# Kernel optimization log

Measured on AMD Instinct MI355X. Metric: run time of the kernel, lower is better.

## Reference

```python
import jax, jax.numpy as jnp
import numpy as np

N, D, H, O, E, K = 131072, 512, 512, 512, 8, 2
LN_EPS = 1e-5


def setup_inputs() -> dict:
    key = jax.random.key(0)
    k0, k1, k2, k3 = jax.random.split(key, 4)
    x = jax.random.normal(k0, (N, D), jnp.float32)
    # gate: nn.init.normal_(weight, 0, 0.1); stored as [D, E] (transposed torch layout)
    Wg = jax.random.normal(k1, (D, E), jnp.float32) * 0.1
    # experts: xavier_uniform for fc1/fc2, LayerNorm gamma=1, beta=0
    b1 = float(np.sqrt(6.0 / (D + H)))
    b2 = float(np.sqrt(6.0 / (H + O)))
    W1 = jax.random.uniform(k2, (E, D, H), jnp.float32, -b1, b1)
    W2 = jax.random.uniform(k3, (E, H, O), jnp.float32, -b2, b2)
    gamma = jnp.ones((E, H), jnp.float32)
    beta = jnp.zeros((E, H), jnp.float32)
    return {"x": x, "Wg": Wg, "W1": W1, "gamma": gamma, "beta": beta, "W2": W2}


def _layer_norm(h, g, b):
    mu = jnp.mean(h, axis=-1, keepdims=True)
    var = jnp.mean(jnp.square(h - mu), axis=-1, keepdims=True)  # biased, as torch LayerNorm
    return (h - mu) * jax.lax.rsqrt(var + LN_EPS) * g + b


def reference(x, Wg, W1, gamma, beta, W2):
    n = x.shape[0]
    # gating: softmax over experts (eval mode: no noise, no dropout)
    gating = jax.nn.softmax(x @ Wg, axis=-1)            # [N, E]
    vals, idx = jax.lax.top_k(gating, K)                # [N, K]
    # F.normalize(p=1): values are positive softmax probs -> divide by L1 sum
    vals = vals / jnp.maximum(jnp.sum(vals, axis=-1, keepdims=True), 1e-12)
    # scatter top-k weights into dense per-expert combine weights [N, E]
    cw = jnp.zeros((n, E), x.dtype).at[jnp.arange(n)[:, None], idx].add(vals)
    out = jnp.zeros((n, W2.shape[-1]), x.dtype)
    for e in range(E):  # small fixed loop over experts
        h = jax.nn.gelu(_layer_norm(x @ W1[e], gamma[e], beta[e]), approximate=False)
        out = out + cw[:, e:e + 1] * (h @ W2[e])
    return out
```

## Files before the change

kernel.cpp:

```cpp
#include <hip/hip_runtime.h>
#include <hip/hip_bf16.h>
#include <stdint.h>

#define NTOK 131072
#define NEXP 8

typedef unsigned short ushortT;
typedef __attribute__((ext_vector_type(4))) float f32x4;
typedef __attribute__((ext_vector_type(8))) short s16x8;
typedef __attribute__((ext_vector_type(8))) __bf16 bf16x8;

__device__ __forceinline__ float bfu2f(unsigned short u){
  union { float f; uint32_t i; } c; c.i = ((uint32_t)u) << 16; return c.f;
}
__device__ __forceinline__ unsigned short f2bfu(float f){
  union { float f; uint32_t i; } c; c.f = f;
  uint32_t x = c.i;
  uint32_t r = (x + 0x7fffu + ((x >> 16) & 1u)) >> 16;
  return (unsigned short)r;
}
__device__ __forceinline__ float gelu_f(float x){
  float u = 0.7978845608028654f * (x + 0.044715f * x * x * x);
  float e = __expf(2.0f * u);
  float t = 1.0f - 2.0f / (e + 1.0f);
  return 0.5f * x * (1.0f + t);
}
__device__ __forceinline__ bf16x8 ldfrag(const void* p){
  s16x8 v = *(const s16x8*)p;
  return __builtin_bit_cast(bf16x8, v);
}

__global__ __launch_bounds__(64) void zero_cursors_kernel(int* __restrict__ cursors){
  if (threadIdx.x < 16) cursors[threadIdx.x] = 0;
}

__global__ __launch_bounds__(256) void prep_w_kernel(const float* __restrict__ W1,
                                                     const float* __restrict__ W2,
                                                     ushortT* __restrict__ W1f,
                                                     ushortT* __restrict__ W2f){
  int bid = blockIdx.x;
  const float* src; ushortT* dst;
  if (bid < 512){ src = W1; dst = W1f; } else { src = W2; dst = W2f; bid -= 512; }
  int e  = bid >> 6;
  int kt = (bid >> 3) & 7;
  int nt = bid & 7;
  __shared__ ushortT tileT[64][68];
  int t = threadIdx.x;
  #pragma unroll
  for (int i = 0; i < 16; i++){
    int idx = t + i*256;
    int r = idx >> 6, c = idx & 63;
    float v = src[((size_t)(e*512 + kt*64 + r))*512 + nt*64 + c];
    tileT[c][r] = f2bfu(v);
  }
  __syncthreads();
  int sub = t >> 6, l = t & 63;
  #pragma unroll
  for (int fo = 0; fo < 2; fo++){
    int fr  = sub + fo*4;
    int nbl = fr >> 1;
    int ks  = fr & 1;
    int nb  = nt*4 + nbl;
    size_t fi = ((size_t)(e*32 + nb))*16 + kt*2 + ks;
    ushortT tmp[8];
    #pragma unroll
    for (int j = 0; j < 8; j++)
      tmp[j] = tileT[nbl*16 + (l & 15)][ks*32 + (l >> 4)*8 + j];
    *(s16x8*)(dst + fi*512 + l*8) = *(s16x8*)tmp;
  }
}

__global__ __launch_bounds__(256) void gating_kernel(const float* __restrict__ x,
                                                     const float* __restrict__ Wg,
                                                     ushortT* __restrict__ xbf,
                                                     int* __restrict__ epair,
                                                     float* __restrict__ wt){
  int l = threadIdx.x & 63;
  int wv = threadIdx.x >> 6;
  f32x4 wgv[16];
  #pragma unroll
  for (int i = 0; i < 8; i++){
    const f32x4* p = (const f32x4*)(Wg + (size_t)(l*8 + i)*8);
    wgv[2*i] = p[0]; wgv[2*i+1] = p[1];
  }
  int tbase = (blockIdx.x * 4 + wv) * 16;
  for (int tt = 0; tt < 16; tt++){
    int t = tbase + tt;
    const f32x4* xr = (const f32x4*)(x + (size_t)t*512 + l*8);
    f32x4 xa = xr[0], xb = xr[1];
    float acc[8];
    #pragma unroll
    for (int e2 = 0; e2 < 8; e2++) acc[e2] = 0.f;
    #pragma unroll
    for (int i = 0; i < 4; i++){
      float xi = xa[i], xj = xb[i];
      #pragma unroll
      for (int e2 = 0; e2 < 4; e2++){
        acc[e2]   += xi * wgv[2*i][e2];
        acc[4+e2] += xi * wgv[2*i+1][e2];
        acc[e2]   += xj * wgv[2*(i+4)][e2];
        acc[4+e2] += xj * wgv[2*(i+4)+1][e2];
      }
    }
    #pragma unroll
    for (int off = 1; off < 64; off <<= 1){
      #pragma unroll
      for (int e2 = 0; e2 < 8; e2++) acc[e2] += __shfl_xor(acc[e2], off);
    }
    int e0 = 0; float v0 = acc[0];
    #pragma unroll
    for (int e2 = 1; e2 < 8; e2++) if (acc[e2] > v0){ v0 = acc[e2]; e0 = e2; }
    int e1 = -1; float v1 = -3.4e38f;
    #pragma unroll
    for (int e2 = 0; e2 < 8; e2++){ if (e2 != e0 && acc[e2] > v1){ v1 = acc[e2]; e1 = e2; } }
    float w0 = 1.f / (1.f + __expf(v1 - v0));
    if (l == 0){
      epair[t] = e0 | (e1 << 4);
      wt[t] = w0;
      wt[NTOK + t] = 1.f - w0;
    }
    s16x8 o;
    #pragma unroll
    for (int j = 0; j < 4; j++){ o[j] = (short)f2bfu(xa[j]); o[4+j] = (short)f2bfu(xb[j]); }
    *(s16x8*)(xbf + (size_t)t*512 + l*8) = o;
  }
}

__global__ __launch_bounds__(256) void scatter_kernel(const int* __restrict__ epair,
                                                      int* __restrict__ cursors,
                                                      int* __restrict__ lists){
  __shared__ int cntL[16]; __shared__ int baseL[16];
  int tid = threadIdx.x;
  if (tid < 16) cntL[tid] = 0;
  __syncthreads();
  int t = blockIdx.x * 256 + tid;
  int p = epair[t];
  int e0 = p & 15, e1 = (p >> 4) & 15;
  int lp0 = atomicAdd(&cntL[e0], 1);
  int lp1 = atomicAdd(&cntL[8 + e1], 1);
  __syncthreads();
  if (tid < 16) baseL[tid] = atomicAdd(&cursors[tid], cntL[tid]);
  __syncthreads();
  lists[(size_t)e0 * NTOK + baseL[e0] + lp0] = t;
  lists[(size_t)(8 + e1) * NTOK + baseL[8 + e1] + lp1] = t;
}

template<int SLOT>
__global__ __launch_bounds__(512, 2) void expert_kernel(
    const ushortT* __restrict__ xbf, const ushortT* __restrict__ W1bf,
    const ushortT* __restrict__ W2bf, const float* __restrict__ gamma,
    const float* __restrict__ beta, const float* __restrict__ wt,
    const int* __restrict__ cursors, const int* __restrict__ lists,
    float* __restrict__ out)
{
  __shared__ ushortT hX[64 * 512];
  __shared__ int   toksL[64];
  __shared__ float wrowL[64];
  __shared__ float wsumL[8][64];
  __shared__ float wsqL[8][64];
  __shared__ float muL[64];
  __shared__ float rsL[64];

  int tid = threadIdx.x;
  int w = tid >> 6;
  int l = tid & 63;

  int bid = (int)blockIdx.x;
  bid = (bid & 7) * 257 + (bid >> 3);

  int e = -1, tile = 0, bacc = 0, cn = 0;
  #pragma unroll
  for (int i = 0; i < 8; i++){
    int c = cursors[SLOT*8 + i];
    int ntl = (c + 63) >> 6;
    if (e < 0 && bid < bacc + ntl){ e = i; tile = bid - bacc; cn = c; }
    bacc += ntl;
  }
  if (e < 0) return;
  int tb = tile * 64;

  if (tid < 64){
    int idx = tb + tid;
    int tok = (idx < cn) ? lists[(size_t)(SLOT*8 + e) * NTOK + idx] : -1;
    toksL[tid] = tok;
    wrowL[tid] = (tok >= 0) ? wt[(size_t)SLOT*NTOK + tok] : 0.f;
  }
  __syncthreads();

  {
    int r = tid >> 3, cs = tid & 7;
    int tokS = toksL[r]; if (tokS < 0) tokS = toksL[0];
    const int4* xrow = (const int4*)(xbf + (size_t)tokS * 512);
    int4 xv[8];
    #pragma unroll
    for (int i = 0; i < 8; i++) xv[i] = xrow[cs + i*8];
    #pragma unroll
    for (int i = 0; i < 8; i++){
      int slot = cs + i*8;
      int ss = slot ^ (r & 7);
      *(int4*)((char*)hX + r*1024 + ss*16) = xv[i];
    }
  }
  __syncthreads();

  const ushortT* w1f = W1bf + ((size_t)(e*32 + w*4))*16*512;
  f32x4 acc[4][4];
  #pragma unroll
  for (int m = 0; m < 4; m++)
    #pragma unroll
    for (int nf = 0; nf < 4; nf++) acc[m][nf] = (f32x4){0.f,0.f,0.f,0.f};

  #pragma unroll 2
  for (int kt = 0; kt < 8; kt++){
    #pragma unroll
    for (int ks = 0; ks < 2; ks++){
      bf16x8 A[4];
      #pragma unroll
      for (int m = 0; m < 4; m++){
        int row = (l & 15) + m*16;
        int slot = kt*8 + ks*4 + (l >> 4);
        A[m] = ldfrag((const char*)hX + row*1024 + (slot ^ (row & 7))*16);
      }
      #pragma unroll
      for (int nf = 0; nf < 4; nf++){
        bf16x8 B = ldfrag(w1f + ((size_t)(nf*16 + kt*2 + ks))*512 + l*8);
        #pragma unroll
        for (int m = 0; m < 4; m++)
          acc[m][nf] = __builtin_amdgcn_mfma_f32_16x16x32_bf16(A[m], B, acc[m][nf], 0, 0, 0);
      }
    }
  }

  #pragma unroll
  for (int m = 0; m < 4; m++){
    #pragma unroll
    for (int j = 0; j < 4; j++){
      float s = acc[m][0][j] + acc[m][1][j] + acc[m][2][j] + acc[m][3][j];
      float q = acc[m][0][j]*acc[m][0][j] + acc[m][1][j]*acc[m][1][j]
              + acc[m][2][j]*acc[m][2][j] + acc[m][3][j]*acc[m][3][j];
      s += __shfl_xor(s, 1); q += __shfl_xor(q, 1);
      s += __shfl_xor(s, 2); q += __shfl_xor(q, 2);
      s += __shfl_xor(s, 4); q += __shfl_xor(q, 4);
      s += __shfl_xor(s, 8); q += __shfl_xor(q, 8);
      if ((l & 15) == 0){
        int row = m*16 + (l >> 4)*4 + j;
        wsumL[w][row] = s;
        wsqL[w][row]  = q;
      }
    }
  }
  __syncthreads();

  if (tid < 64){
    float s = 0.f, q = 0.f;
    #pragma unroll
    for (int i = 0; i < 8; i++){ s += wsumL[i][tid]; q += wsqL[i][tid]; }
    float mu = s * (1.f/512.f);
    float var = q * (1.f/512.f) - mu*mu;
    muL[tid] = mu;
    rsL[tid] = rsqrtf(var + 1e-5f);
  }
  __syncthreads();

  {
    float g[4], b[4];
    #pragma unroll
    for (int nf = 0; nf < 4; nf++){
      int col = w*64 + nf*16 + (l & 15);
      g[nf] = gamma[e*512 + col];
      b[nf] = beta [e*512 + col];
    }
    #pragma unroll
    for (int m = 0; m < 4; m++){
      #pragma unroll
      for (int j = 0; j < 4; j++){
        int row = m*16 + (l >> 4)*4 + j;
        float mu = muL[row], rs = rsL[row];
        #pragma unroll
        for (int nf = 0; nf < 4; nf++){
          int col = w*64 + nf*16 + (l & 15);
          float v = (acc[m][nf][j] - mu) * rs * g[nf] + b[nf];
          v = gelu_f(v);
          int ss = (col >> 3) ^ (row & 7);
          *(ushortT*)((char*)hX + row*1024 + ss*16 + (col & 7)*2) = f2bfu(v);
        }
      }
    }
  }
  __syncthreads();

  const ushortT* w2f = W2bf + ((size_t)(e*32 + w*4))*16*512;
  #pragma unroll
  for (int m = 0; m < 4; m++)
    #pragma unroll
    for (int nf = 0; nf < 4; nf++) acc[m][nf] = (f32x4){0.f,0.f,0.f,0.f};

  #pragma unroll 2
  for (int kt = 0; kt < 8; kt++){
    #pragma unroll
    for (int ks = 0; ks < 2; ks++){
      bf16x8 A[4];
      #pragma unroll
      for (int m = 0; m < 4; m++){
        int row = (l & 15) + m*16;
        int slot = kt*8 + ks*4 + (l >> 4);
        A[m] = ldfrag((const char*)hX + row*1024 + (slot ^ (row & 7))*16);
      }
      #pragma unroll
      for (int nf = 0; nf < 4; nf++){
        bf16x8 B = ldfrag(w2f + ((size_t)(nf*16 + kt*2 + ks))*512 + l*8);
        #pragma unroll
        for (int m = 0; m < 4; m++)
          acc[m][nf] = __builtin_amdgcn_mfma_f32_16x16x32_bf16(A[m], B, acc[m][nf], 0, 0, 0);
      }
    }
  }

  #pragma unroll
  for (int m = 0; m < 4; m++){
    #pragma unroll
    for (int j = 0; j < 4; j++){
      int row = m*16 + (l >> 4)*4 + j;
      int tok = toksL[row];
      if (tok >= 0){
        float wr = wrowL[row];
        #pragma unroll
        for (int nf = 0; nf < 4; nf++){
          int col = w*64 + nf*16 + (l & 15);
          float val = acc[m][nf][j] * wr;
          float* p = out + (size_t)tok*512 + col;
          if (SLOT == 0) *p = val; else *p += val;
        }
      }
    }
  }
}

extern "C" void kernel_launch(void* const* d_in, const int* in_sizes, int n_in,
                              void* d_out, int out_size, void* d_ws, size_t ws_size,
                              hipStream_t stream){
  const float* x     = (const float*)d_in[0];
  const float* Wg    = (const float*)d_in[1];
  const float* W1    = (const float*)d_in[2];
  const float* gamma = (const float*)d_in[3];
  const float* beta  = (const float*)d_in[4];
  const float* W2    = (const float*)d_in[5];
  float* out = (float*)d_out;

  char* ws = (char*)d_ws;
  size_t off = 0;
  ushortT* xbf   = (ushortT*)(ws + off); off += (size_t)NTOK*512*2;
  ushortT* W1bf  = (ushortT*)(ws + off); off += (size_t)8*512*512*2;
  ushortT* W2bf  = (ushortT*)(ws + off); off += (size_t)8*512*512*2;
  int*     lists = (int*)(ws + off);     off += (size_t)16*NTOK*4;
  float*   wtp   = (float*)(ws + off);   off += (size_t)2*NTOK*4;
  int*     epair = (int*)(ws + off);     off += (size_t)NTOK*4;
  int*     cursors = (int*)(ws + off);   off += 256;

  zero_cursors_kernel<<<1, 64, 0, stream>>>(cursors);
  prep_w_kernel<<<1024, 256, 0, stream>>>(W1, W2, W1bf, W2bf);
  gating_kernel<<<NTOK/64, 256, 0, stream>>>(x, Wg, xbf, epair, wtp);
  scatter_kernel<<<NTOK/256, 256, 0, stream>>>(epair, cursors, lists);
  expert_kernel<0><<<2056, 512, 0, stream>>>(xbf, W1bf, W2bf, gamma, beta, wtp, cursors, lists, out);
  expert_kernel<1><<<2056, 512, 0, stream>>>(xbf, W1bf, W2bf, gamma, beta, wtp, cursors, lists, out);
}
```

Measured before the change: 639.8 us.

## Raise expert kernel occupancy and double-buffer weight fragment loads in GEMMs

Raises launch bounds from 2 to 4 blocks per CU. Both expert GEMMs become fully unrolled loops that prefetch the next step's B fragments from global memory while the current MFMAs run, using precomputed swizzled LDS offsets. The token gather now reads the list directly instead of waiting on a barrier after the shared token table is filled, and gamma/beta are loaded per use rather than held in registers. Doubling occupancy caps registers per thread more tightly, which may cause spills given the 64-float accumulator plus double-buffered fragments. LDS use of about 64KB per block may also keep four blocks from fitting on a CU.

```diff
diff --git a/kernel.cpp b/kernel.cpp
--- a/kernel.cpp
+++ b/kernel.cpp
@@ -146,7 +146,7 @@
 }
 
 template<int SLOT>
-__global__ __launch_bounds__(512, 2) void expert_kernel(
+__global__ __launch_bounds__(512, 4) void expert_kernel(
     const ushortT* __restrict__ xbf, const ushortT* __restrict__ W1bf,
     const ushortT* __restrict__ W2bf, const float* __restrict__ gamma,
     const float* __restrict__ beta, const float* __restrict__ wt,
@@ -178,56 +178,75 @@
   }
   if (e < 0) return;
   int tb = tile * 64;
+  const int* lbase = lists + (size_t)(SLOT*8 + e) * NTOK;
 
   if (tid < 64){
     int idx = tb + tid;
-    int tok = (idx < cn) ? lists[(size_t)(SLOT*8 + e) * NTOK + idx] : -1;
+    int tok = (idx < cn) ? lbase[idx] : -1;
     toksL[tid] = tok;
     wrowL[tid] = (tok >= 0) ? wt[(size_t)SLOT*NTOK + tok] : 0.f;
   }
-  __syncthreads();
 
   {
     int r = tid >> 3, cs = tid & 7;
-    int tokS = toksL[r]; if (tokS < 0) tokS = toksL[0];
+    int idx = tb + r; if (idx >= cn) idx = tb;
+    int tokS = lbase[idx];
     const int4* xrow = (const int4*)(xbf + (size_t)tokS * 512);
-    int4 xv[8];
-    #pragma unroll
-    for (int i = 0; i < 8; i++) xv[i] = xrow[cs + i*8];
-    #pragma unroll
-    for (int i = 0; i < 8; i++){
-      int slot = cs + i*8;
-      int ss = slot ^ (r & 7);
-      *(int4*)((char*)hX + r*1024 + ss*16) = xv[i];
-    }
-  }
-  __syncthreads();
+    #pragma unroll
+    for (int half = 0; half < 2; half++){
+      int4 xv[4];
+      #pragma unroll
+      for (int i = 0; i < 4; i++) xv[i] = xrow[cs + (half*4 + i)*8];
+      #pragma unroll
+      for (int i = 0; i < 4; i++){
+        int slot = cs + (half*4 + i)*8;
+        int ss = slot ^ (r & 7);
+        *(int4*)((char*)hX + r*1024 + ss*16) = xv[i];
+      }
+    }
+  }
+  __syncthreads();
+
+  const int aB0 = (l & 15)*1024 + ((((l >> 4)    ) ^ (l & 7)) << 4);
+  const int aB1 = (l & 15)*1024 + (((4 + (l >> 4)) ^ (l & 7)) << 4);
+  const char* Xp = (const char*)hX;
 
   const ushortT* w1f = W1bf + ((size_t)(e*32 + w*4))*16*512;
+  const ushortT* w2f = W2bf + ((size_t)(e*32 + w*4))*16*512;
+
   f32x4 acc[4][4];
+
+#define LOADB(dst, wf, s_) { \
+    _Pragma("unroll") \
+    for (int nf = 0; nf < 4; nf++) \
+      dst[nf] = ldfrag((wf) + ((nf*16 + (s_)) << 9) + (l << 3)); }
+#define LOADA(dst, s_) { \
+    const int ab_ = ((s_) & 1) ? aB1 : aB0; \
+    _Pragma("unroll") \
+    for (int m = 0; m < 4; m++) \
+      dst[m] = ldfrag(Xp + ab_ + m*16384 + ((s_) >> 1)*128); }
+#define MFMAS(Aa, Bb) { \
+    _Pragma("unroll") \
+    for (int nf = 0; nf < 4; nf++) \
+      _Pragma("unroll") \
+      for (int m = 0; m < 4; m++) \
+        acc[m][nf] = __builtin_amdgcn_mfma_f32_16x16x32_bf16(Aa[m], Bb[nf], acc[m][nf], 0, 0, 0); }
+
   #pragma unroll
   for (int m = 0; m < 4; m++)
     #pragma unroll
     for (int nf = 0; nf < 4; nf++) acc[m][nf] = (f32x4){0.f,0.f,0.f,0.f};
-
-  #pragma unroll 2
-  for (int kt = 0; kt < 8; kt++){
-    #pragma unroll
-    for (int ks = 0; ks < 2; ks++){
-      bf16x8 A[4];
-      #pragma unroll
-      for (int m = 0; m < 4; m++){
-        int row = (l & 15) + m*16;
-        int slot = kt*8 + ks*4 + (l >> 4);
-        A[m] = ldfrag((const char*)hX + row*1024 + (slot ^ (row & 7))*16);
-      }
-      #pragma unroll
-      for (int nf = 0; nf < 4; nf++){
-        bf16x8 B = ldfrag(w1f + ((size_t)(nf*16 + kt*2 + ks))*512 + l*8);
-        #pragma unroll
-        for (int m = 0; m < 4; m++)
-          acc[m][nf] = __builtin_amdgcn_mfma_f32_16x16x32_bf16(A[m], B, acc[m][nf], 0, 0, 0);
-      }
+  {
+    bf16x8 Ba[4], Bb[4];
+    LOADB(Ba, w1f, 0);
+    #pragma unroll
+    for (int s = 0; s < 16; s += 2){
+      { bf16x8 A[4]; LOADA(A, s);
+        LOADB(Bb, w1f, s+1);
+        MFMAS(A, Ba); }
+      { bf16x8 A[4]; LOADA(A, s+1);
+        if (s+2 < 16) LOADB(Ba, w1f, s+2);
+        MFMAS(A, Bb); }
     }
   }
 
@@ -263,13 +282,6 @@
   __syncthreads();
 
   {
-    float g[4], b[4];
-    #pragma unroll
-    for (int nf = 0; nf < 4; nf++){
-      int col = w*64 + nf*16 + (l & 15);
-      g[nf] = gamma[e*512 + col];
-      b[nf] = beta [e*512 + col];
-    }
     #pragma unroll
     for (int m = 0; m < 4; m++){
       #pragma unroll
@@ -279,7 +291,9 @@
         #pragma unroll
         for (int nf = 0; nf < 4; nf++){
           int col = w*64 + nf*16 + (l & 15);
-          float v = (acc[m][nf][j] - mu) * rs * g[nf] + b[nf];
+          float g = gamma[e*512 + col];
+          float b = beta [e*512 + col];
+          float v = (acc[m][nf][j] - mu) * rs * g + b;
           v = gelu_f(v);
           int ss = (col >> 3) ^ (row & 7);
           *(ushortT*)((char*)hX + row*1024 + ss*16 + (col & 7)*2) = f2bfu(v);
@@ -289,30 +303,21 @@
   }
   __syncthreads();
 
-  const ushortT* w2f = W2bf + ((size_t)(e*32 + w*4))*16*512;
   #pragma unroll
   for (int m = 0; m < 4; m++)
     #pragma unroll
     for (int nf = 0; nf < 4; nf++) acc[m][nf] = (f32x4){0.f,0.f,0.f,0.f};
-
-  #pragma unroll 2
-  for (int kt = 0; kt < 8; kt++){
-    #pragma unroll
-    for (int ks = 0; ks < 2; ks++){
-      bf16x8 A[4];
-      #pragma unroll
-      for (int m = 0; m < 4; m++){
-        int row = (l & 15) + m*16;
-        int slot = kt*8 + ks*4 + (l >> 4);
-        A[m] = ldfrag((const char*)hX + row*1024 + (slot ^ (row & 7))*16);
-      }
-      #pragma unroll
-      for (int nf = 0; nf < 4; nf++){
-        bf16x8 B = ldfrag(w2f + ((size_t)(nf*16 + kt*2 + ks))*512 + l*8);
-        #pragma unroll
-        for (int m = 0; m < 4; m++)
-          acc[m][nf] = __builtin_amdgcn_mfma_f32_16x16x32_bf16(A[m], B, acc[m][nf], 0, 0, 0);
-      }
+  {
+    bf16x8 Ba[4], Bb[4];
+    LOADB(Ba, w2f, 0);
+    #pragma unroll
+    for (int s = 0; s < 16; s += 2){
+      { bf16x8 A[4]; LOADA(A, s);
+        LOADB(Bb, w2f, s+1);
+        MFMAS(A, Ba); }
+      { bf16x8 A[4]; LOADA(A, s+1);
+        if (s+2 < 16) LOADB(Ba, w2f, s+2);
+        MFMAS(A, Bb); }
     }
   }
 
@@ -334,6 +339,9 @@
       }
     }
   }
+#undef LOADB
+#undef LOADA
+#undef MFMAS
 }
 
 extern "C" void kernel_launch(void* const* d_in, const int* in_sizes, int n_in,
```

Result: slower. 748.4 us (+17.0%).

## Split fused expert kernel into tiled GEMM1, LayerNorm-GELU, and GEMM2 passes

Applied to the files above, without the earlier changes.

Replaces the single fused per-expert kernel with three kernels. The first GEMM is tiled 128 rows x 128 cols with double-buffered direct global-to-LDS loads, and it writes raw bf16 activations plus partial row statistics to a workspace. A separate kernel applies LayerNorm and GELU in place. A second tiled GEMM reads the activations back and scatters the weighted output. The aim is better operand reuse, load/compute overlap and occupancy, paid for by extra HBM round-trips of the hidden activations and more kernel launches.

```diff
diff --git a/kernel.cpp b/kernel.cpp
--- a/kernel.cpp
+++ b/kernel.cpp
@@ -4,6 +4,7 @@
 
 #define NTOK 131072
 #define NEXP 8
+#define HPAD 132096
 
 typedef unsigned short ushortT;
 typedef __attribute__((ext_vector_type(4))) float f32x4;
@@ -29,6 +30,10 @@
   s16x8 v = *(const s16x8*)p;
   return __builtin_bit_cast(bf16x8, v);
 }
+
+#define GLOAD16(g_, l_) \
+  __builtin_amdgcn_global_load_lds((const __attribute__((address_space(1))) uint32_t*)(g_), \
+                                   (__attribute__((address_space(3))) uint32_t*)(l_), 16, 0, 0)
 
 __global__ __launch_bounds__(64) void zero_cursors_kernel(int* __restrict__ cursors){
   if (threadIdx.x < 16) cursors[threadIdx.x] = 0;
@@ -146,188 +151,253 @@
 }
 
 template<int SLOT>
-__global__ __launch_bounds__(512, 2) void expert_kernel(
+__global__ __launch_bounds__(256, 3) void g1_kernel(
     const ushortT* __restrict__ xbf, const ushortT* __restrict__ W1bf,
-    const ushortT* __restrict__ W2bf, const float* __restrict__ gamma,
-    const float* __restrict__ beta, const float* __restrict__ wt,
     const int* __restrict__ cursors, const int* __restrict__ lists,
-    float* __restrict__ out)
+    ushortT* __restrict__ hraw, float* __restrict__ stats)
 {
-  __shared__ ushortT hX[64 * 512];
-  __shared__ int   toksL[64];
-  __shared__ float wrowL[64];
-  __shared__ float wsumL[8][64];
-  __shared__ float wsqL[8][64];
-  __shared__ float muL[64];
-  __shared__ float rsL[64];
-
-  int tid = threadIdx.x;
-  int w = tid >> 6;
-  int l = tid & 63;
-
-  int bid = (int)blockIdx.x;
-  bid = (bid & 7) * 257 + (bid >> 3);
+  __shared__ ushortT Abuf[2][4096];
+  __shared__ ushortT Bbuf[2][4096];
+  __shared__ int toksL[128];
+
+  int tid = threadIdx.x, w = tid >> 6, l = tid & 63;
+  int braw = (int)blockIdx.x;
+  int bid = (braw & 7)*516 + (braw >> 3);
+  int t128 = bid >> 2, nt = bid & 3;
 
   int e = -1, tile = 0, bacc = 0, cn = 0;
   #pragma unroll
   for (int i = 0; i < 8; i++){
     int c = cursors[SLOT*8 + i];
-    int ntl = (c + 63) >> 6;
-    if (e < 0 && bid < bacc + ntl){ e = i; tile = bid - bacc; cn = c; }
+    int ntl = (c + 127) >> 7;
+    if (e < 0 && t128 < bacc + ntl){ e = i; tile = t128 - bacc; cn = c; }
     bacc += ntl;
   }
   if (e < 0) return;
-  int tb = tile * 64;
-
+  const int* lbase = lists + (size_t)(SLOT*8 + e) * NTOK;
+
+  if (tid < 128){
+    int idx = tile*128 + tid;
+    toksL[tid] = lbase[(idx < cn) ? idx : tile*128];
+  }
+  __syncthreads();
+
+  int rA0 = tid >> 2, rA1 = 64 + (tid >> 2), cA = tid & 3;
+  int swzA = (cA ^ (rA0 & 3)) << 4;
+  const char* srcA0 = (const char*)(xbf + (size_t)toksL[rA0]*512) + swzA;
+  const char* srcA1 = (const char*)(xbf + (size_t)toksL[rA1]*512) + swzA;
+  const char* srcB0 = (const char*)W1bf + ((size_t)((e*32 + nt*8 + w    )*16))*1024 + (l << 4);
+  const char* srcB1 = (const char*)W1bf + ((size_t)((e*32 + nt*8 + w + 4)*16))*1024 + (l << 4);
+
+#define STAGE_(b_, s_) { \
+    GLOAD16(srcA0 + (size_t)(s_)*64,   &Abuf[b_][w*512]); \
+    GLOAD16(srcA1 + (size_t)(s_)*64,   &Abuf[b_][2048 + w*512]); \
+    GLOAD16(srcB0 + (size_t)(s_)*1024, &Bbuf[b_][w*512]); \
+    GLOAD16(srcB1 + (size_t)(s_)*1024, &Bbuf[b_][2048 + w*512]); }
+
+  int wr = w >> 1, wc = w & 1;
+  int aswz = ((l >> 4) ^ (l & 3)) << 4;
+  int ab0 = (wr*64 + (l & 15))*64 + aswz;
+  int bb0 = (wc*4)*1024 + (l << 4);
+
+  f32x4 acc[4][4];
+  #pragma unroll
+  for (int m = 0; m < 4; m++)
+    #pragma unroll
+    for (int nf = 0; nf < 4; nf++) acc[m][nf] = (f32x4){0.f,0.f,0.f,0.f};
+
+  STAGE_(0, 0);
+  __syncthreads();
+  for (int s = 0; s < 16; s++){
+    int b = s & 1;
+    if (s < 15) STAGE_(b ^ 1, s + 1);
+    bf16x8 A[4], B[4];
+    #pragma unroll
+    for (int m = 0; m < 4; m++)  A[m]  = ldfrag((const char*)&Abuf[b][0] + ab0 + m*1024);
+    #pragma unroll
+    for (int nf = 0; nf < 4; nf++) B[nf] = ldfrag((const char*)&Bbuf[b][0] + bb0 + nf*1024);
+    #pragma unroll
+    for (int nf = 0; nf < 4; nf++)
+      #pragma unroll
+      for (int m = 0; m < 4; m++)
+        acc[m][nf] = __builtin_amdgcn_mfma_f32_16x16x32_bf16(A[m], B[nf], acc[m][nf], 0, 0, 0);
+    __syncthreads();
+  }
+#undef STAGE_
+
+  #pragma unroll
+  for (int m = 0; m < 4; m++){
+    #pragma unroll
+    for (int j = 0; j < 4; j++){
+      float s1 = acc[m][0][j] + acc[m][1][j] + acc[m][2][j] + acc[m][3][j];
+      float q1 = acc[m][0][j]*acc[m][0][j] + acc[m][1][j]*acc[m][1][j]
+               + acc[m][2][j]*acc[m][2][j] + acc[m][3][j]*acc[m][3][j];
+      s1 += __shfl_xor(s1, 1); q1 += __shfl_xor(q1, 1);
+      s1 += __shfl_xor(s1, 2); q1 += __shfl_xor(q1, 2);
+      s1 += __shfl_xor(s1, 4); q1 += __shfl_xor(q1, 4);
+      s1 += __shfl_xor(s1, 8); q1 += __shfl_xor(q1, 8);
+      int r = wr*64 + m*16 + (l >> 4)*4 + j;
+      int i = tile*128 + r;
+      if (i < cn){
+        size_t grow = (size_t)t128*128 + r;
+        if ((l & 15) == 0){
+          float2 v; v.x = s1; v.y = q1;
+          *((float2*)stats + grow*8 + (nt*2 + wc)) = v;
+        }
+        #pragma unroll
+        for (int nf = 0; nf < 4; nf++)
+          hraw[grow*512 + nt*128 + wc*64 + nf*16 + (l & 15)] = f2bfu(acc[m][nf][j]);
+      }
+    }
+  }
+}
+
+template<int SLOT>
+__global__ __launch_bounds__(256) void lng_kernel(
+    const int* __restrict__ cursors, const float* __restrict__ stats,
+    const float* __restrict__ gamma, const float* __restrict__ beta,
+    ushortT* __restrict__ hraw)
+{
+  __shared__ float gL[512], bL[512], muL[64], rsL[64];
+  int tid = threadIdx.x;
+  int braw = (int)blockIdx.x;
+  int t64 = (braw & 7)*258 + (braw >> 3);
+  int e = -1, bacc = 0, tstart = 0, cn = 0;
+  #pragma unroll
+  for (int i = 0; i < 8; i++){
+    int c = cursors[SLOT*8 + i];
+    int ntl = 2*((c + 127) >> 7);
+    if (e < 0 && t64 < bacc + ntl){ e = i; tstart = bacc; cn = c; }
+    bacc += ntl;
+  }
+  if (e < 0) return;
+  gL[tid] = gamma[e*512 + tid]; gL[tid+256] = gamma[e*512 + 256 + tid];
+  bL[tid] = beta [e*512 + tid]; bL[tid+256] = beta [e*512 + 256 + tid];
   if (tid < 64){
-    int idx = tb + tid;
-    int tok = (idx < cn) ? lists[(size_t)(SLOT*8 + e) * NTOK + idx] : -1;
-    toksL[tid] = tok;
-    wrowL[tid] = (tok >= 0) ? wt[(size_t)SLOT*NTOK + tok] : 0.f;
-  }
-  __syncthreads();
-
-  {
-    int r = tid >> 3, cs = tid & 7;
-    int tokS = toksL[r]; if (tokS < 0) tokS = toksL[0];
-    const int4* xrow = (const int4*)(xbf + (size_t)tokS * 512);
-    int4 xv[8];
-    #pragma unroll
-    for (int i = 0; i < 8; i++) xv[i] = xrow[cs + i*8];
-    #pragma unroll
-    for (int i = 0; i < 8; i++){
-      int slot = cs + i*8;
-      int ss = slot ^ (r & 7);
-      *(int4*)((char*)hX + r*1024 + ss*16) = xv[i];
-    }
-  }
-  __syncthreads();
-
-  const ushortT* w1f = W1bf + ((size_t)(e*32 + w*4))*16*512;
-  f32x4 acc[4][4];
-  #pragma unroll
-  for (int m = 0; m < 4; m++)
-    #pragma unroll
-    for (int nf = 0; nf < 4; nf++) acc[m][nf] = (f32x4){0.f,0.f,0.f,0.f};
-
-  #pragma unroll 2
-  for (int kt = 0; kt < 8; kt++){
-    #pragma unroll
-    for (int ks = 0; ks < 2; ks++){
-      bf16x8 A[4];
-      #pragma unroll
-      for (int m = 0; m < 4; m++){
-        int row = (l & 15) + m*16;
-        int slot = kt*8 + ks*4 + (l >> 4);
-        A[m] = ldfrag((const char*)hX + row*1024 + (slot ^ (row & 7))*16);
-      }
-      #pragma unroll
-      for (int nf = 0; nf < 4; nf++){
-        bf16x8 B = ldfrag(w1f + ((size_t)(nf*16 + kt*2 + ks))*512 + l*8);
-        #pragma unroll
-        for (int m = 0; m < 4; m++)
-          acc[m][nf] = __builtin_amdgcn_mfma_f32_16x16x32_bf16(A[m], B, acc[m][nf], 0, 0, 0);
-      }
-    }
-  }
-
-  #pragma unroll
-  for (int m = 0; m < 4; m++){
-    #pragma unroll
-    for (int j = 0; j < 4; j++){
-      float s = acc[m][0][j] + acc[m][1][j] + acc[m][2][j] + acc[m][3][j];
-      float q = acc[m][0][j]*acc[m][0][j] + acc[m][1][j]*acc[m][1][j]
-              + acc[m][2][j]*acc[m][2][j] + acc[m][3][j]*acc[m][3][j];
-      s += __shfl_xor(s, 1); q += __shfl_xor(q, 1);
-      s += __shfl_xor(s, 2); q += __shfl_xor(q, 2);
-      s += __shfl_xor(s, 4); q += __shfl_xor(q, 4);
-      s += __shfl_xor(s, 8); q += __shfl_xor(q, 8);
-      if ((l & 15) == 0){
-        int row = m*16 + (l >> 4)*4 + j;
-        wsumL[w][row] = s;
-        wsqL[w][row]  = q;
-      }
-    }
-  }
-  __syncthreads();
-
-  if (tid < 64){
+    size_t grow = (size_t)t64*64 + tid;
+    const float2* sp = (const float2*)stats + grow*8;
     float s = 0.f, q = 0.f;
     #pragma unroll
-    for (int i = 0; i < 8; i++){ s += wsumL[i][tid]; q += wsqL[i][tid]; }
+    for (int k = 0; k < 8; k++){ float2 v = sp[k]; s += v.x; q += v.y; }
     float mu = s * (1.f/512.f);
     float var = q * (1.f/512.f) - mu*mu;
     muL[tid] = mu;
     rsL[tid] = rsqrtf(var + 1e-5f);
   }
   __syncthreads();
-
-  {
-    float g[4], b[4];
-    #pragma unroll
-    for (int nf = 0; nf < 4; nf++){
-      int col = w*64 + nf*16 + (l & 15);
-      g[nf] = gamma[e*512 + col];
-      b[nf] = beta [e*512 + col];
-    }
-    #pragma unroll
-    for (int m = 0; m < 4; m++){
-      #pragma unroll
-      for (int j = 0; j < 4; j++){
-        int row = m*16 + (l >> 4)*4 + j;
-        float mu = muL[row], rs = rsL[row];
+  int lrow0 = (t64 - tstart)*64;
+  for (int v = tid; v < 4096; v += 256){
+    int r = v >> 6, cv = v & 63;
+    size_t grow = (size_t)t64*64 + r;
+    ushortT* p = hraw + grow*512 + cv*8;
+    s16x8 o;
+    if (lrow0 + r < cn){
+      s16x8 u = *(s16x8*)p;
+      float mu = muL[r], rs = rsL[r];
+      #pragma unroll
+      for (int j = 0; j < 8; j++){
+        int col = cv*8 + j;
+        float val = (bfu2f((unsigned short)u[j]) - mu)*rs*gL[col] + bL[col];
+        o[j] = (short)f2bfu(gelu_f(val));
+      }
+    } else {
+      #pragma unroll
+      for (int j = 0; j < 8; j++) o[j] = 0;
+    }
+    *(s16x8*)p = o;
+  }
+}
+
+template<int SLOT>
+__global__ __launch_bounds__(256, 3) void g2_kernel(
+    const ushortT* __restrict__ hraw, const ushortT* __restrict__ W2bf,
+    const float* __restrict__ wt, const int* __restrict__ cursors,
+    const int* __restrict__ lists, float* __restrict__ out)
+{
+  __shared__ ushortT Abuf[2][4096];
+  __shared__ ushortT Bbuf[2][4096];
+  __shared__ int   toksL[128];
+  __shared__ float wrowL[128];
+
+  int tid = threadIdx.x, w = tid >> 6, l = tid & 63;
+  int braw = (int)blockIdx.x;
+  int bid = (braw & 7)*516 + (braw >> 3);
+  int t128 = bid >> 2, nt = bid & 3;
+
+  int e = -1, tile = 0, bacc = 0, cn = 0;
+  #pragma unroll
+  for (int i = 0; i < 8; i++){
+    int c = cursors[SLOT*8 + i];
+    int ntl = (c + 127) >> 7;
+    if (e < 0 && t128 < bacc + ntl){ e = i; tile = t128 - bacc; cn = c; }
+    bacc += ntl;
+  }
+  if (e < 0) return;
+  const int* lbase = lists + (size_t)(SLOT*8 + e) * NTOK;
+
+  if (tid < 128){
+    int idx = tile*128 + tid;
+    int tok = lbase[(idx < cn) ? idx : tile*128];
+    toksL[tid] = tok;
+    wrowL[tid] = wt[(size_t)SLOT*NTOK + tok];
+  }
+
+  int rA0 = tid >> 2, rA1 = 64 + (tid >> 2), cA = tid & 3;
+  int swzA = (cA ^ (rA0 & 3)) << 4;
+  const char* srcA0 = (const char*)(hraw + ((size_t)t128*128 + rA0)*512) + swzA;
+  const char* srcA1 = (const char*)(hraw + ((size_t)t128*128 + rA1)*512) + swzA;
+  const char* srcB0 = (const char*)W2bf + ((size_t)((e*32 + nt*8 + w    )*16))*1024 + (l << 4);
+  const char* srcB1 = (const char*)W2bf + ((size_t)((e*32 + nt*8 + w + 4)*16))*1024 + (l << 4);
+
+#define STAGE_(b_, s_) { \
+    GLOAD16(srcA0 + (size_t)(s_)*64,   &Abuf[b_][w*512]); \
+    GLOAD16(srcA1 + (size_t)(s_)*64,   &Abuf[b_][2048 + w*512]); \
+    GLOAD16(srcB0 + (size_t)(s_)*1024, &Bbuf[b_][w*512]); \
+    GLOAD16(srcB1 + (size_t)(s_)*1024, &Bbuf[b_][2048 + w*512]); }
+
+  int wr = w >> 1, wc = w & 1;
+  int aswz = ((l >> 4) ^ (l & 3)) << 4;
+  int ab0 = (wr*64 + (l & 15))*64 + aswz;
+  int bb0 = (wc*4)*1024 + (l << 4);
+
+  f32x4 acc[4][4];
+  #pragma unroll
+  for (int m = 0; m < 4; m++)
+    #pragma unroll
+    for (int nf = 0; nf < 4; nf++) acc[m][nf] = (f32x4){0.f,0.f,0.f,0.f};
+
+  STAGE_(0, 0);
+  __syncthreads();
+  for (int s = 0; s < 16; s++){
+    int b = s & 1;
+    if (s < 15) STAGE_(b ^ 1, s + 1);
+    bf16x8 A[4], B[4];
+    #pragma unroll
+    for (int m = 0; m < 4; m++)  A[m]  = ldfrag((const char*)&Abuf[b][0] + ab0 + m*1024);
+    #pragma unroll
+    for (int nf = 0; nf < 4; nf++) B[nf] = ldfrag((const char*)&Bbuf[b][0] + bb0 + nf*1024);
+    #pragma unroll
+    for (int nf = 0; nf < 4; nf++)
+      #pragma unroll
+      for (int m = 0; m < 4; m++)
+        acc[m][nf] = __builtin_amdgcn_mfma_f32_16x16x32_bf16(A[m], B[nf], acc[m][nf], 0, 0, 0);
+    __syncthreads();
+  }
+#undef STAGE_
+
+  #pragma unroll
+  for (int m = 0; m < 4; m++){
+    #pragma unroll
+    for (int j = 0; j < 4; j++){
+      int r = wr*64 + m*16 + (l >> 4)*4 + j;
+      int i = tile*128 + r;
+      if (i < cn){
+        int tok = toksL[r];
+        float wr_ = wrowL[r];
         #pragma unroll
         for (int nf = 0; nf < 4; nf++){
-          int col = w*64 + nf*16 + (l & 15);
-          float v = (acc[m][nf][j] - mu) * rs * g[nf] + b[nf];
-          v = gelu_f(v);
-          int ss = (col >> 3) ^ (row & 7);
-          *(ushortT*)((char*)hX + row*1024 + ss*16 + (col & 7)*2) = f2bfu(v);
-        }
-      }
-    }
-  }
-  __syncthreads();
-
-  const ushortT* w2f = W2bf + ((size_t)(e*32 + w*4))*16*512;
-  #pragma unroll
-  for (int m = 0; m < 4; m++)
-    #pragma unroll
-    for (int nf = 0; nf < 4; nf++) acc[m][nf] = (f32x4){0.f,0.f,0.f,0.f};
-
-  #pragma unroll 2
-  for (int kt = 0; kt < 8; kt++){
-    #pragma unroll
-    for (int ks = 0; ks < 2; ks++){
-      bf16x8 A[4];
-      #pragma unroll
-      for (int m = 0; m < 4; m++){
-        int row = (l & 15) + m*16;
-        int slot = kt*8 + ks*4 + (l >> 4);
-        A[m] = ldfrag((const char*)hX + row*1024 + (slot ^ (row & 7))*16);
-      }
-      #pragma unroll
-      for (int nf = 0; nf < 4; nf++){
-        bf16x8 B = ldfrag(w2f + ((size_t)(nf*16 + kt*2 + ks))*512 + l*8);
-        #pragma unroll
-        for (int m = 0; m < 4; m++)
-          acc[m][nf] = __builtin_amdgcn_mfma_f32_16x16x32_bf16(A[m], B, acc[m][nf], 0, 0, 0);
-      }
-    }
-  }
-
-  #pragma unroll
-  for (int m = 0; m < 4; m++){
-    #pragma unroll
-    for (int j = 0; j < 4; j++){
-      int row = m*16 + (l >> 4)*4 + j;
-      int tok = toksL[row];
-      if (tok >= 0){
-        float wr = wrowL[row];
-        #pragma unroll
-        for (int nf = 0; nf < 4; nf++){
-          int col = w*64 + nf*16 + (l & 15);
-          float val = acc[m][nf][j] * wr;
+          int col = nt*128 + wc*64 + nf*16 + (l & 15);
+          float val = acc[m][nf][j] * wr_;
           float* p = out + (size_t)tok*512 + col;
           if (SLOT == 0) *p = val; else *p += val;
         }
@@ -356,11 +426,19 @@
   float*   wtp   = (float*)(ws + off);   off += (size_t)2*NTOK*4;
   int*     epair = (int*)(ws + off);     off += (size_t)NTOK*4;
   int*     cursors = (int*)(ws + off);   off += 256;
+  float*   stats = (float*)(ws + off);   off += (size_t)HPAD*8*2*4;
+  ushortT* hraw  = (ushortT*)(ws + off); off += (size_t)HPAD*512*2;
 
   zero_cursors_kernel<<<1, 64, 0, stream>>>(cursors);
   prep_w_kernel<<<1024, 256, 0, stream>>>(W1, W2, W1bf, W2bf);
   gating_kernel<<<NTOK/64, 256, 0, stream>>>(x, Wg, xbf, epair, wtp);
   scatter_kernel<<<NTOK/256, 256, 0, stream>>>(epair, cursors, lists);
-  expert_kernel<0><<<2056, 512, 0, stream>>>(xbf, W1bf, W2bf, gamma, beta, wtp, cursors, lists, out);
-  expert_kernel<1><<<2056, 512, 0, stream>>>(xbf, W1bf, W2bf, gamma, beta, wtp, cursors, lists, out);
-}
+
+  g1_kernel<0><<<4128, 256, 0, stream>>>(xbf, W1bf, cursors, lists, hraw, stats);
+  lng_kernel<0><<<2064, 256, 0, stream>>>(cursors, stats, gamma, beta, hraw);
+  g2_kernel<0><<<4128, 256, 0, stream>>>(hraw, W2bf, wtp, cursors, lists, out);
+
+  g1_kernel<1><<<4128, 256, 0, stream>>>(xbf, W1bf, cursors, lists, hraw, stats);
+  lng_kernel<1><<<2064, 256, 0, stream>>>(cursors, stats, gamma, beta, hraw);
+  g2_kernel<1><<<4128, 256, 0, stream>>>(hraw, W2bf, wtp, cursors, lists, out);
+}
```

New measurement: 848.2 us. 32.6% more time.
